# Optimization experiments

Measured on AMD Instinct MI355X. Metric: run time of the kernel, lower is better.

Reference implementation:

```python
import jax, jax.numpy as jnp
import numpy as np

D, H, F, L, V = 768, 4, 1024, 3, 10000
B, TLAB, S = 16, 513, 197
SCALE = 0.02


def setup_inputs() -> dict:
    key = jax.random.key(0)
    ks = jax.random.split(key, 16)
    inp = {
        'labels': jax.random.randint(ks[0], (B, TLAB), 0, V),
        'vision_feats': jax.random.normal(ks[1], (B, S, D), jnp.float32),
        'vis_proj_w': jax.random.normal(ks[2], (D, D), jnp.float32) * SCALE,
        'vis_proj_b': jnp.zeros((D,), jnp.float32),
        'tok_emb': jax.random.normal(ks[3], (V, D), jnp.float32) * SCALE,
        'pos_emb': jax.random.normal(ks[4], (1, 512, D), jnp.float32) * SCALE,
        'sa_w': jax.random.normal(ks[5], (L, 3 * D, D), jnp.float32) * SCALE,
        'sa_b': jnp.zeros((L, 3 * D), jnp.float32),
        'sa_out_w': jax.random.normal(ks[6], (L, D, D), jnp.float32) * SCALE,
        'sa_out_b': jnp.zeros((L, D), jnp.float32),
        'ca_w': jax.random.normal(ks[7], (L, 3 * D, D), jnp.float32) * SCALE,
        'ca_b': jnp.zeros((L, 3 * D), jnp.float32),
        'ca_out_w': jax.random.normal(ks[8], (L, D, D), jnp.float32) * SCALE,
        'ca_out_b': jnp.zeros((L, D), jnp.float32),
        'ln1_g': jnp.ones((L, D), jnp.float32), 'ln1_b': jnp.zeros((L, D), jnp.float32),
        'ln2_g': jnp.ones((L, D), jnp.float32), 'ln2_b': jnp.zeros((L, D), jnp.float32),
        'ln3_g': jnp.ones((L, D), jnp.float32), 'ln3_b': jnp.zeros((L, D), jnp.float32),
        'ff1_w': jax.random.normal(ks[9], (L, F, D), jnp.float32) * SCALE,
        'ff1_b': jnp.zeros((L, F), jnp.float32),
        'ff2_w': jax.random.normal(ks[10], (L, D, F), jnp.float32) * SCALE,
        'ff2_b': jnp.zeros((L, D), jnp.float32),
        'out_w': jax.random.normal(ks[11], (V, D), jnp.float32) * SCALE,
        'out_b': jnp.zeros((V,), jnp.float32),
    }
    return inp


def layer_norm(x, g, b, eps=1e-5):
    m = jnp.mean(x, axis=-1, keepdims=True)
    v = jnp.var(x, axis=-1, keepdims=True)
    return (x - m) / jnp.sqrt(v + eps) * g + b


def mha(qx, kx, vx, w, b, ow, ob, mask):
    # torch nn.MultiheadAttention with packed in_proj [3D, D]
    d = qx.shape[-1]
    hd = d // H
    q = qx @ w[:d].T + b[:d]
    k = kx @ w[d:2 * d].T + b[d:2 * d]
    v = vx @ w[2 * d:].T + b[2 * d:]
    def split(t):
        return t.reshape(t.shape[0], t.shape[1], H, hd).transpose(0, 2, 1, 3)
    q, k, v = split(q), split(k), split(v)  # [B,H,T,hd]
    s = jnp.einsum('bhqd,bhkd->bhqk', q, k) / jnp.sqrt(jnp.asarray(hd, qx.dtype))
    if mask is not None:
        s = s + mask
    a = jax.nn.softmax(s, axis=-1)
    o = jnp.einsum('bhqk,bhkd->bhqd', a, v)
    o = o.transpose(0, 2, 1, 3).reshape(qx.shape[0], qx.shape[1], d)
    return o @ ow.T + ob


def decode(labels, vision_feats, vis_proj_w, vis_proj_b, tok_emb, pos_emb,
           sa_w, sa_b, sa_out_w, sa_out_b, ca_w, ca_b, ca_out_w, ca_out_b,
           ln1_g, ln1_b, ln2_g, ln2_b, ln3_g, ln3_b,
           ff1_w, ff1_b, ff2_w, ff2_b, out_w, out_b):
    mem = vision_feats @ vis_proj_w.T + vis_proj_b          # [B,S,D]
    tgt_tok = labels[:, :-1]                                # [B,T] T=512
    T = tgt_tok.shape[1]
    x = tok_emb[tgt_tok] + pos_emb[:, :T, :]                # [B,T,D]
    # causal additive mask (teacher-forced loop == single full causal pass)
    mask = jnp.where(jnp.tril(jnp.ones((T, T), bool)), 0.0, -jnp.inf).astype(x.dtype)
    for l in range(L):
        x = layer_norm(x + mha(x, x, x, sa_w[l], sa_b[l], sa_out_w[l], sa_out_b[l], mask), ln1_g[l], ln1_b[l])
        x = layer_norm(x + mha(x, mem, mem, ca_w[l], ca_b[l], ca_out_w[l], ca_out_b[l], None), ln2_g[l], ln2_b[l])
        ff = jax.nn.relu(x @ ff1_w[l].T + ff1_b[l]) @ ff2_w[l].T + ff2_b[l]
        x = layer_norm(x + ff, ln3_g[l], ln3_b[l])
    return x @ out_w.T + out_b                              # [B,T,V]


def reference(labels, vision_feats, vis_proj_w, vis_proj_b, tok_emb, pos_emb,
              sa_w, sa_b, sa_out_w, sa_out_b, ca_w, ca_b, ca_out_w, ca_out_b,
              ln1_g, ln1_b, ln2_g, ln2_b, ln3_g, ln3_b,
              ff1_w, ff1_b, ff2_w, ff2_b, out_w, out_b):
    logits = decode(labels, vision_feats, vis_proj_w, vis_proj_b, tok_emb, pos_emb,
                    sa_w, sa_b, sa_out_w, sa_out_b, ca_w, ca_b, ca_out_w, ca_out_b,
                    ln1_g, ln1_b, ln2_g, ln2_b, ln3_g, ln3_b,
                    ff1_w, ff1_b, ff2_w, ff2_b, out_w, out_b)
    return (logits, labels[:, 1:])
```

## Files before the change

kernel.cpp:

```cpp
#include <hip/hip_runtime.h>
#include <hip/hip_fp8.h>

typedef unsigned short u16;
typedef __bf16 bf16x8 __attribute__((ext_vector_type(8)));
typedef float f32x4 __attribute__((ext_vector_type(4)));
typedef unsigned short u16x8 __attribute__((ext_vector_type(8)));
typedef unsigned short u16x4 __attribute__((ext_vector_type(4)));
typedef long i64;

typedef __attribute__((address_space(3))) u16 lds_u16_t;
typedef __attribute__((address_space(1))) const u16 glb_u16_t;
typedef __attribute__((address_space(3))) unsigned char lds_u8_t;
typedef __attribute__((address_space(1))) const unsigned char glb_u8_t;

__device__ __forceinline__ u16 f2bf(float f) {
    union { float f; unsigned u; } v; v.f = f;
    unsigned r = v.u + 0x7FFFu + ((v.u >> 16) & 1u);
    return (u16)(r >> 16);
}
__device__ __forceinline__ float bf2f(u16 h) {
    union { unsigned u; float f; } v; v.u = ((unsigned)h) << 16; return v.f;
}
__device__ __forceinline__ unsigned char f2e4m3(float f) {
    __hip_fp8_e4m3 h(f);
    return (unsigned char)h.__x;
}

struct CastQ { const float* s[9]; unsigned char* d[9]; long n4[9]; float mul[9]; };
__global__ __launch_bounds__(256) void castq_kernel(CastQ a) {
    int seg = blockIdx.z;
    const float* s = a.s[seg];
    unsigned char* d = a.d[seg];
    long n4 = a.n4[seg];
    float mul = a.mul[seg];
    long i = (long)blockIdx.x * 256 + threadIdx.x;
    long stride = (long)gridDim.x * 256;
    for (; i < n4; i += stride) {
        float4 f = reinterpret_cast<const float4*>(s)[i];
        uchar4 o;
        o.x = f2e4m3(f.x * mul); o.y = f2e4m3(f.y * mul);
        o.z = f2e4m3(f.z * mul); o.w = f2e4m3(f.w * mul);
        reinterpret_cast<uchar4*>(d)[i] = o;
    }
}

__global__ __launch_bounds__(256) void embed_kernel(
    const int* __restrict__ labels, const float* __restrict__ tok_emb,
    const float* __restrict__ pos_emb, u16* __restrict__ xb,
    unsigned char* __restrict__ xq, float* __restrict__ lab_out)
{
    int wid = threadIdx.x >> 6, lane = threadIdx.x & 63;
    int r = blockIdx.x * 4 + wid;
    int b = r >> 9, t = r & 511;
    int tok = labels[b * 513 + t];
    if (lane == 0) lab_out[r] = (float)labels[b * 513 + t + 1];
    const float* te = tok_emb + (long)tok * 768;
    const float* pe = pos_emb + (long)t * 768;
    u16* xo = xb + (long)r * 768;
    unsigned char* qo = xq + (long)r * 768;
    int base = lane * 12;
#pragma unroll
    for (int c = 0; c < 3; c++) {
        float4 a = *reinterpret_cast<const float4*>(te + base + c * 4);
        float4 p = *reinterpret_cast<const float4*>(pe + base + c * 4);
        float v0 = a.x + p.x, v1 = a.y + p.y, v2 = a.z + p.z, v3 = a.w + p.w;
        ushort4 o; o.x = f2bf(v0); o.y = f2bf(v1); o.z = f2bf(v2); o.w = f2bf(v3);
        *reinterpret_cast<ushort4*>(xo + base + c * 4) = o;
        uchar4 q; q.x = f2e4m3(v0); q.y = f2e4m3(v1); q.z = f2e4m3(v2); q.w = f2e4m3(v3);
        *reinterpret_cast<uchar4*>(qo + base + c * 4) = q;
    }
}

template<int OUT>
__global__ __launch_bounds__(256, 4) void gemmT(
    const u16* __restrict__ A, int lda, long sAb, long sAh,
    const u16* __restrict__ W, int ldw, long sWb, long sWh,
    void* __restrict__ C, int ldc, long sCb, long sCh,
    int M, int N, int K, int NH)
{
    __shared__ __align__(16) u16 As0[128 * 32];
    __shared__ __align__(16) u16 As1[128 * 32];
    __shared__ __align__(16) u16 Bs0[128 * 32];
    __shared__ __align__(16) u16 Bs1[128 * 32];

    int z = blockIdx.z, zb = z / NH, zh = z % NH;
    const u16* Ap = A + (long)zb * sAb + (long)zh * sAh;
    const u16* Wp = W + (long)zb * sWb + (long)zh * sWh;
    long coff = (long)zb * sCb + (long)zh * sCh;

    int gx = (int)gridDim.x, gy = (int)gridDim.y;
    int nwg = gx * gy;
    int orig = (int)(blockIdx.y * gridDim.x + blockIdx.x);
    int q = nwg >> 3, r = nwg & 7;
    int xcd = orig & 7, loc = orig >> 3;
    int wg = (xcd < r ? xcd * (q + 1) : r * (q + 1) + (xcd - r) * q) + loc;
    int full = 8 * gy;
    int nsc = (gx + 7) >> 3;
    int sc = wg / full; if (sc > nsc - 1) sc = nsc - 1;
    int rem = wg - sc * full;
    int wdt = gx - sc * 8; if (wdt > 8) wdt = 8;
    int by = rem / wdt, bx = sc * 8 + rem % wdt;

    int m0 = by * 128, n0 = bx * 128;
    int tid = threadIdx.x, wid = tid >> 6, lane = tid & 63;
    int wr = (wid >> 1) * 64, wc = (wid & 1) * 64;
    int fr = lane & 15, fk = (lane >> 4) * 8;

    int li0 = wid * 64 + lane;
    int li1 = li0 + 256;
    int r0 = li0 >> 2, c0 = (li0 & 3) * 8;
    int r1 = li1 >> 2, c1 = (li1 & 3) * 8;
    long aoff0 = (long)min(m0 + r0, M - 1) * lda + c0;
    long aoff1 = (long)min(m0 + r1, M - 1) * lda + c1;
    long woff0 = (long)min(n0 + r0, N - 1) * ldw + c0;
    long woff1 = (long)min(n0 + r1, N - 1) * ldw + c1;
    char* a0base = (char*)As0 + wid * 1024;
    char* a1base = (char*)As1 + wid * 1024;
    char* b0base = (char*)Bs0 + wid * 1024;
    char* b1base = (char*)Bs1 + wid * 1024;

    f32x4 acc[4][4] = {};

    auto stage = [&](char* ab, char* bb, int kt) {
        int k0 = kt * 32;
        __builtin_amdgcn_global_load_lds((glb_u16_t*)(Ap + aoff0 + k0), (lds_u16_t*)ab, 16, 0, 0);
        __builtin_amdgcn_global_load_lds((glb_u16_t*)(Ap + aoff1 + k0), (lds_u16_t*)(ab + 4096), 16, 0, 0);
        __builtin_amdgcn_global_load_lds((glb_u16_t*)(Wp + woff0 + k0), (lds_u16_t*)bb, 16, 0, 0);
        __builtin_amdgcn_global_load_lds((glb_u16_t*)(Wp + woff1 + k0), (lds_u16_t*)(bb + 4096), 16, 0, 0);
    };
    auto compute = [&](const u16* as, const u16* bs) {
        bf16x8 af[4], bw[4];
#pragma unroll
        for (int m = 0; m < 4; m++)
            af[m] = *reinterpret_cast<const bf16x8*>(&as[(wr + m * 16 + fr) * 32 + fk]);
#pragma unroll
        for (int n = 0; n < 4; n++)
            bw[n] = *reinterpret_cast<const bf16x8*>(&bs[(wc + n * 16 + fr) * 32 + fk]);
#pragma unroll
        for (int m = 0; m < 4; m++)
#pragma unroll
            for (int n = 0; n < 4; n++)
                acc[m][n] = __builtin_amdgcn_mfma_f32_16x16x32_bf16(af[m], bw[n], acc[m][n], 0, 0, 0);
    };

    int nt = K >> 5;
    stage(a0base, b0base, 0);
    __syncthreads();
    for (int t = 0; t < nt; t += 2) {
        stage(a1base, b1base, t + 1);
        compute(As0, Bs0);
        __syncthreads();
        if (t + 2 < nt) stage(a0base, b0base, t + 2);
        compute(As1, Bs1);
        __syncthreads();
    }

    int crow = (lane >> 4) * 4;
#pragma unroll
    for (int m = 0; m < 4; m++) {
#pragma unroll
        for (int n = 0; n < 4; n++) {
            int col = n0 + wc + n * 16 + fr;
            if (col >= N) continue;
            int rbase = m0 + wr + m * 16 + crow;
#pragma unroll
            for (int rr = 0; rr < 4; rr++) {
                int row = rbase + rr;
                if (row >= M) continue;
                float v = acc[m][n][rr];
                long idx = coff + (long)row * ldc + col;
                if (OUT == 1) ((u16*)C)[idx] = f2bf(v);
                else          ((unsigned char*)C)[idx] = f2e4m3(v);
            }
        }
    }
}

template<int OUT, int RELU, int BM, int FUSEVT>
__global__ __launch_bounds__(256, 4) void gemm8(
    const unsigned char* __restrict__ A, int lda,
    const unsigned char* __restrict__ W, int ldw,
    const float* __restrict__ bias, float outscale,
    void* __restrict__ C, int ldc, u16* __restrict__ vt,
    int M, int N, int K)
{
    constexpr int NREP = (BM == 128) ? 4 : 2;
    constexpr int AHALF = (BM == 128) ? 4096 : 2048;
    __shared__ __align__(16) unsigned char As0[BM * 64];
    __shared__ __align__(16) unsigned char As1[BM * 64];
    __shared__ __align__(16) unsigned char Bs0[128 * 64];
    __shared__ __align__(16) unsigned char Bs1[128 * 64];

    int gx = (int)gridDim.x, gy = (int)gridDim.y;
    int nwg = gx * gy;
    int orig = (int)(blockIdx.y * gridDim.x + blockIdx.x);
    int q = nwg >> 3, r = nwg & 7;
    int xcd = orig & 7, loc = orig >> 3;
    int wg = (xcd < r ? xcd * (q + 1) : r * (q + 1) + (xcd - r) * q) + loc;
    int full = 8 * gy;
    int nsc = (gx + 7) >> 3;
    int sc = wg / full; if (sc > nsc - 1) sc = nsc - 1;
    int rem = wg - sc * full;
    int wdt = gx - sc * 8; if (wdt > 8) wdt = 8;
    int by = rem / wdt, bx = sc * 8 + rem % wdt;

    int m0 = by * BM, n0 = bx * 128;
    int tid = threadIdx.x, wid = tid >> 6, lane = tid & 63;
    int wr = (BM == 128) ? (wid >> 1) * 64 : 0;
    int wc = (BM == 128) ? (wid & 1) * 64 : wid * 32;
    int fr = lane & 15, gk = (lane >> 4) * 8;

    int li0 = wid * 64 + lane;
    int rsW = li0 >> 1, csW = li0 & 1;
    int kcW = ((csW ^ (rsW >> 2)) & 1) << 4;
    long woff = (long)min(n0 + rsW, N - 1) * ldw + kcW;
    long aoff;
    if constexpr (BM == 128) {
        aoff = (long)min(m0 + rsW, M - 1) * lda + kcW;
    } else {
        int halfA = li0 >> 7;
        int rsA = (li0 >> 1) & 63, csA = li0 & 1;
        int kcA = ((csA ^ (rsA >> 2)) & 1) << 4;
        aoff = (long)min(m0 + rsA, M - 1) * lda + halfA * 32 + kcA;
    }
    char* a0base = (char*)As0 + wid * 1024;
    char* a1base = (char*)As1 + wid * 1024;
    char* b0base = (char*)Bs0 + wid * 1024;
    char* b1base = (char*)Bs1 + wid * 1024;

    f32x4 acc[4][NREP] = {};

    auto stage = [&](char* ab, char* bb, int kt) {
        int k0 = kt * 64;
        if constexpr (BM == 128) {
            __builtin_amdgcn_global_load_lds((glb_u8_t*)(A + aoff + k0), (lds_u8_t*)ab, 16, 0, 0);
            __builtin_amdgcn_global_load_lds((glb_u8_t*)(A + aoff + k0 + 32), (lds_u8_t*)(ab + 4096), 16, 0, 0);
        } else {
            __builtin_amdgcn_global_load_lds((glb_u8_t*)(A + aoff + k0), (lds_u8_t*)ab, 16, 0, 0);
        }
        __builtin_amdgcn_global_load_lds((glb_u8_t*)(W + woff + k0), (lds_u8_t*)bb, 16, 0, 0);
        __builtin_amdgcn_global_load_lds((glb_u8_t*)(W + woff + k0 + 32), (lds_u8_t*)(bb + 4096), 16, 0, 0);
    };
    int cg = gk >> 4, go = gk & 15;
    auto compute = [&](const unsigned char* as, const unsigned char* bs) {
        i64 af[4][2], bw[NREP][2];
#pragma unroll
        for (int m = 0; m < 4; m++) {
            int rr2 = wr + m * 16 + fr;
            int off = rr2 * 32 + (((cg ^ (rr2 >> 2)) & 1) << 4) + go;
            af[m][0] = *reinterpret_cast<const i64*>(as + off);
            af[m][1] = *reinterpret_cast<const i64*>(as + AHALF + off);
        }
#pragma unroll
        for (int n = 0; n < NREP; n++) {
            int rr2 = wc + n * 16 + fr;
            int off = rr2 * 32 + (((cg ^ (rr2 >> 2)) & 1) << 4) + go;
            bw[n][0] = *reinterpret_cast<const i64*>(bs + off);
            bw[n][1] = *reinterpret_cast<const i64*>(bs + 4096 + off);
        }
#pragma unroll
        for (int ks = 0; ks < 2; ks++)
#pragma unroll
            for (int m = 0; m < 4; m++)
#pragma unroll
                for (int n = 0; n < NREP; n++)
                    acc[m][n] = __builtin_amdgcn_mfma_f32_16x16x32_fp8_fp8(
                        af[m][ks], bw[n][ks], acc[m][n], 0, 0, 0);
    };

    int nt = K >> 6;
    stage(a0base, b0base, 0);
    __syncthreads();
    for (int t = 0; t < nt; t += 2) {
        stage(a1base, b1base, t + 1);
        compute(As0, Bs0);
        __syncthreads();
        if (t + 2 < nt) stage(a0base, b0base, t + 2);
        compute(As1, Bs1);
        __syncthreads();
    }

    int crow = (lane >> 4) * 4;
#pragma unroll
    for (int m = 0; m < 4; m++) {
#pragma unroll
        for (int n = 0; n < NREP; n++) {
            int col = n0 + wc + n * 16 + fr;
            if (col >= N) continue;
            float bv = bias ? bias[col] : 0.f;
            int rbase = m0 + wr + m * 16 + crow;
            float vv[4];
#pragma unroll
            for (int rr = 0; rr < 4; rr++) {
                int row = rbase + rr;
                if (row >= M) continue;
                float v = acc[m][n][rr] * outscale + bv;
                if (RELU) v = fmaxf(v, 0.f);
                vv[rr] = v;
                long idx = (long)row * ldc + col;
                if (OUT == 0)      ((float*)C)[idx] = v;
                else if (OUT == 1) ((u16*)C)[idx] = f2bf(v);
                else               ((unsigned char*)C)[idx] = f2e4m3(v);
            }
            if constexpr (FUSEVT) {
                if (col >= 1536) {
                    int tt = col - 1536;
                    int h = tt / 192, d = tt - h * 192;
                    int b = rbase >> 9, k0 = rbase & 511;
                    ushort4 o;
                    o.x = f2bf(vv[0]); o.y = f2bf(vv[1]); o.z = f2bf(vv[2]); o.w = f2bf(vv[3]);
                    *reinterpret_cast<ushort4*>(vt + ((long)((b << 2) + h) * 192 + d) * 512 + k0) = o;
                }
            }
        }
    }
}

__global__ __launch_bounds__(256) void transpose_pad(
    const u16* __restrict__ V, long sVb, long sVh, int ldv, int NH,
    u16* __restrict__ VT, long sVT, int rowsIn, int Kp)
{
    __shared__ u16 tile[32][33];
    int z = blockIdx.z, zb = z / NH, zh = z % NH;
    const u16* Vp = V + (long)zb * sVb + (long)zh * sVh;
    int k0 = blockIdx.x * 32, d0 = blockIdx.y * 32;
#pragma unroll
    for (int i = 0; i < 4; i++) {
        int k = k0 + threadIdx.y + i * 8;
        int d = d0 + threadIdx.x;
        tile[threadIdx.y + i * 8][threadIdx.x] = (k < rowsIn) ? Vp[(long)k * ldv + d] : (u16)0;
    }
    __syncthreads();
    u16* Op = VT + (long)z * sVT;
#pragma unroll
    for (int i = 0; i < 4; i++) {
        int d = d0 + threadIdx.y + i * 8;
        int k = k0 + threadIdx.x;
        Op[(long)d * Kp + k] = tile[threadIdx.x][threadIdx.y + i * 8];
    }
}

template<int CPL, int CAUSAL>
__global__ __launch_bounds__(256) void softmax2(
    const u16* __restrict__ S, u16* __restrict__ P,
    int ld_in, int valid_in, int ld_out, float scale)
{
    int wid = threadIdx.x >> 6, lane = threadIdx.x & 63;
    long r = (long)blockIdx.x * 4 + wid;
    int q = (int)(r & 511);
    int valid = CAUSAL ? (q + 1) : valid_in;
    const u16* srow = S + r * (long)ld_in;
    u16* prow = P + r * (long)ld_out;
    int base = lane * CPL;
    float v[CPL];
    if constexpr (CPL == 8) {
        u16x8 x = *reinterpret_cast<const u16x8*>(srow + base);
#pragma unroll
        for (int j = 0; j < 8; j++) v[j] = bf2f(x[j]);
    } else {
        u16x4 x = *reinterpret_cast<const u16x4*>(srow + base);
#pragma unroll
        for (int j = 0; j < 4; j++) v[j] = bf2f(x[j]);
    }
    float mx = -3e38f;
#pragma unroll
    for (int j = 0; j < CPL; j++) {
        v[j] *= scale;
        if (base + j < valid) mx = fmaxf(mx, v[j]);
    }
#pragma unroll
    for (int o = 32; o; o >>= 1) mx = fmaxf(mx, __shfl_xor(mx, o, 64));
    float e[CPL], s = 0.f;
#pragma unroll
    for (int j = 0; j < CPL; j++) {
        e[j] = (base + j < valid) ? __expf(v[j] - mx) : 0.f;
        s += e[j];
    }
#pragma unroll
    for (int o = 32; o; o >>= 1) s += __shfl_xor(s, o, 64);
    float inv = 1.f / s;
    if constexpr (CPL == 8) {
        u16x8 o8;
#pragma unroll
        for (int j = 0; j < 8; j++) o8[j] = f2bf(e[j] * inv);
        *reinterpret_cast<u16x8*>(prow + base) = o8;
    } else {
        u16x4 o4;
#pragma unroll
        for (int j = 0; j < 4; j++) o4[j] = f2bf(e[j] * inv);
        *reinterpret_cast<u16x4*>(prow + base) = o4;
    }
}

__global__ __launch_bounds__(256) void ln_kernel(
    const u16* __restrict__ xin, const u16* __restrict__ subb,
    const float* __restrict__ g, const float* __restrict__ bta,
    u16* __restrict__ xout, unsigned char* __restrict__ q8)
{
    int wid = threadIdx.x >> 6, lane = threadIdx.x & 63;
    long r = (long)blockIdx.x * 4 + wid;
    const u16* a = xin + r * 768;
    const u16* s = subb + r * 768;
    int base = lane * 12;
    float v[12];
    float sum = 0.f;
#pragma unroll
    for (int c = 0; c < 3; c++) {
        ushort4 av = *reinterpret_cast<const ushort4*>(a + base + c * 4);
        ushort4 sv = *reinterpret_cast<const ushort4*>(s + base + c * 4);
        v[c*4+0] = bf2f(av.x) + bf2f(sv.x);
        v[c*4+1] = bf2f(av.y) + bf2f(sv.y);
        v[c*4+2] = bf2f(av.z) + bf2f(sv.z);
        v[c*4+3] = bf2f(av.w) + bf2f(sv.w);
        sum += v[c*4+0] + v[c*4+1] + v[c*4+2] + v[c*4+3];
    }
#pragma unroll
    for (int o = 32; o; o >>= 1) sum += __shfl_xor(sum, o, 64);
    float mean = sum * (1.f / 768.f);
    float vs = 0.f;
#pragma unroll
    for (int j = 0; j < 12; j++) { float t = v[j] - mean; vs += t * t; }
#pragma unroll
    for (int o = 32; o; o >>= 1) vs += __shfl_xor(vs, o, 64);
    float rstd = rsqrtf(vs * (1.f / 768.f) + 1e-5f);
    u16* xo = xout + r * 768;
    unsigned char* qo = q8 + r * 768;
#pragma unroll
    for (int c = 0; c < 3; c++) {
        float4 gv = *reinterpret_cast<const float4*>(g + base + c * 4);
        float4 bv = *reinterpret_cast<const float4*>(bta + base + c * 4);
        float y0 = (v[c*4+0] - mean) * rstd * gv.x + bv.x;
        float y1 = (v[c*4+1] - mean) * rstd * gv.y + bv.y;
        float y2 = (v[c*4+2] - mean) * rstd * gv.z + bv.z;
        float y3 = (v[c*4+3] - mean) * rstd * gv.w + bv.w;
        ushort4 o; o.x = f2bf(y0); o.y = f2bf(y1); o.z = f2bf(y2); o.w = f2bf(y3);
        *reinterpret_cast<ushort4*>(xo + base + c * 4) = o;
        uchar4 qb; qb.x = f2e4m3(y0); qb.y = f2e4m3(y1); qb.z = f2e4m3(y2); qb.w = f2e4m3(y3);
        *reinterpret_cast<uchar4*>(qo + base + c * 4) = qb;
    }
}

template<int OUT>
static void gbat(hipStream_t st,
    const u16* A, int lda, long sAb, long sAh,
    const u16* W, int ldw, long sWb, long sWh,
    void* C, int ldc, long sCb, long sCh,
    int M, int N, int K, int Z, int NH) {
    dim3 g((N + 127) / 128, (M + 127) / 128, Z), b(256, 1, 1);
    gemmT<OUT><<<g,b,0,st>>>(A,lda,sAb,sAh,W,ldw,sWb,sWh,C,ldc,sCb,sCh,M,N,K,NH);
}
template<int OUT, int RELU, int BM>
static void g8(hipStream_t st, const unsigned char* A, int lda, const unsigned char* W, int ldw,
               const float* bias, void* C, int ldc, int M, int N, int K) {
    dim3 g((N + 127) / 128, (M + BM - 1) / BM, 1), b(256, 1, 1);
    gemm8<OUT,RELU,BM,0><<<g,b,0,st>>>(A,lda,W,ldw,bias,1.f/256.f,C,ldc,nullptr,M,N,K);
}
static void g8qkv(hipStream_t st, const unsigned char* A, const unsigned char* W,
                  const float* bias, u16* C, u16* vt) {
    dim3 g(18, 64, 1), b(256, 1, 1);
    gemm8<1,0,128,1><<<g,b,0,st>>>(A,768,W,768,bias,1.f/256.f,C,2304,vt,8192,2304,768);
}

extern "C" void kernel_launch(void* const* d_in, const int* in_sizes, int n_in,
                              void* d_out, int out_size, void* d_ws, size_t ws_size,
                              hipStream_t stream)
{
    const int*   labels = (const int*)  d_in[0];
    const float* vision = (const float*)d_in[1];
    const float* vpw    = (const float*)d_in[2];
    const float* vpb    = (const float*)d_in[3];
    const float* temb   = (const float*)d_in[4];
    const float* pemb   = (const float*)d_in[5];
    const float* saw    = (const float*)d_in[6];
    const float* sab    = (const float*)d_in[7];
    const float* saow   = (const float*)d_in[8];
    const float* saob   = (const float*)d_in[9];
    const float* caw    = (const float*)d_in[10];
    const float* cab    = (const float*)d_in[11];
    const float* caow   = (const float*)d_in[12];
    const float* caob   = (const float*)d_in[13];
    const float* ln1g   = (const float*)d_in[14];
    const float* ln1b   = (const float*)d_in[15];
    const float* ln2g   = (const float*)d_in[16];
    const float* ln2b   = (const float*)d_in[17];
    const float* ln3g   = (const float*)d_in[18];
    const float* ln3b   = (const float*)d_in[19];
    const float* f1w    = (const float*)d_in[20];
    const float* f1b    = (const float*)d_in[21];
    const float* f2w    = (const float*)d_in[22];
    const float* f2b    = (const float*)d_in[23];
    const float* ow     = (const float*)d_in[24];
    const float* ob     = (const float*)d_in[25];
    (void)in_sizes; (void)n_in; (void)out_size;

    char* p = (char*)d_ws;
    auto alloc = [&](long elems, int esz) -> char* {
        char* r = p; p += ((long)elems * esz + 255) & ~255L; return r;
    };
    unsigned char* w8_sa  = (unsigned char*)alloc(3L*2304*768, 1);
    unsigned char* w8_ca  = (unsigned char*)alloc(3L*2304*768, 1);
    unsigned char* w8_sao = (unsigned char*)alloc(3L*768*768, 1);
    unsigned char* w8_cao = (unsigned char*)alloc(3L*768*768, 1);
    unsigned char* w8_f1  = (unsigned char*)alloc(3L*1024*768, 1);
    unsigned char* w8_f2  = (unsigned char*)alloc(3L*768*1024, 1);
    unsigned char* w8_ow  = (unsigned char*)alloc(10000L*768, 1);
    unsigned char* w8_vp  = (unsigned char*)alloc(768L*768, 1);
    unsigned char* vis8   = (unsigned char*)alloc(3152L*768, 1);
    unsigned char* mem8   = (unsigned char*)alloc(3152L*768, 1);
    unsigned char* xq     = (unsigned char*)alloc(8192L*768, 1);
    unsigned char* h8     = (unsigned char*)alloc(8192L*1024, 1);
    unsigned char* attn8  = (unsigned char*)alloc(8192L*768, 1);
    u16* xb   = (u16*)alloc(8192L*768, 2);
    u16* qkv  = (u16*)alloc(8192L*2304, 2);
    u16* q_bf = qkv;
    u16* kv_bf = qkv + 8192L*768;
    u16* scb  = (u16*)alloc(64L*512*512, 2);
    u16* pr   = (u16*)alloc(64L*512*512, 2);
    u16* vt   = (u16*)alloc(64L*192*512, 2);
    u16* subb = (u16*)alloc(8192L*768, 2);
    if ((size_t)(p - (char*)d_ws) > ws_size) return;

    CastQ cq;
    cq.s[0] = saw;    cq.d[0] = w8_sa;  cq.n4[0] = 3L*2304*768/4;  cq.mul[0] = 256.f;
    cq.s[1] = caw;    cq.d[1] = w8_ca;  cq.n4[1] = 3L*2304*768/4;  cq.mul[1] = 256.f;
    cq.s[2] = saow;   cq.d[2] = w8_sao; cq.n4[2] = 3L*768*768/4;   cq.mul[2] = 256.f;
    cq.s[3] = caow;   cq.d[3] = w8_cao; cq.n4[3] = 3L*768*768/4;   cq.mul[3] = 256.f;
    cq.s[4] = f1w;    cq.d[4] = w8_f1;  cq.n4[4] = 3L*1024*768/4;  cq.mul[4] = 256.f;
    cq.s[5] = f2w;    cq.d[5] = w8_f2;  cq.n4[5] = 3L*768*1024/4;  cq.mul[5] = 256.f;
    cq.s[6] = ow;     cq.d[6] = w8_ow;  cq.n4[6] = 10000L*768/4;   cq.mul[6] = 256.f;
    cq.s[7] = vpw;    cq.d[7] = w8_vp;  cq.n4[7] = 768L*768/4;     cq.mul[7] = 256.f;
    cq.s[8] = vision; cq.d[8] = vis8;   cq.n4[8] = 3152L*768/4;    cq.mul[8] = 1.f;
    castq_kernel<<<dim3(512, 1, 9), dim3(256), 0, stream>>>(cq);

    embed_kernel<<<dim3(2048), dim3(256), 0, stream>>>(labels, temb, pemb, xb, xq,
                                                       (float*)d_out + 81920000L);

    g8<2,0,64>(stream, vis8, 768, w8_vp, 768, vpb, mem8, 768, 3152, 768, 768);

    const float scale = 0.07216878364870323f;

    for (int l = 0; l < 3; l++) {
        g8qkv(stream, xq, w8_sa + (long)l*2304*768, sab + l*2304, qkv, vt);
        gbat<1>(stream, qkv, 2304, 512L*2304, 192, qkv + 768, 2304, 512L*2304, 192,
                scb, 512, 4L*512*512, 512L*512, 512, 512, 192, 64, 4);
        softmax2<8,1><<<dim3(8192), dim3(256), 0, stream>>>(scb, pr, 512, 512, 512, scale);
        gbat<2>(stream, pr, 512, 4L*512*512, 512L*512, vt, 512, 4L*192*512, 192L*512,
                attn8, 768, 512L*768, 192, 512, 192, 512, 64, 4);
        g8<1,0,64>(stream, attn8, 768, w8_sao + (long)l*768*768, 768,
                   saob + l*768, subb, 768, 8192, 768, 768);
        ln_kernel<<<dim3(2048), dim3(256), 0, stream>>>(xb, subb, ln1g + l*768, ln1b + l*768,
                                                        xb, xq);

        g8<1,0,64>(stream, xq, 768, w8_ca + (long)l*2304*768, 768,
                   cab + l*2304, q_bf, 768, 8192, 768, 768);
        g8<1,0,64>(stream, mem8, 768, w8_ca + (long)l*2304*768 + 768L*768, 768,
                   cab + l*2304 + 768, kv_bf, 1536, 3152, 1536, 768);
        transpose_pad<<<dim3(8,6,64), dim3(32,8), 0, stream>>>(
            kv_bf + 768, 197L*1536, 192L, 1536, 4, vt, 192L*256, 197, 256);
        gbat<1>(stream, q_bf, 768, 512L*768, 192, kv_bf, 1536, 197L*1536, 192,
                scb, 224, 4L*512*224, 512L*224, 512, 197, 192, 64, 4);
        softmax2<4,0><<<dim3(8192), dim3(256), 0, stream>>>(scb, pr, 224, 197, 256, scale);
        gbat<2>(stream, pr, 256, 4L*512*256, 512L*256, vt, 256, 4L*192*256, 192L*256,
                attn8, 768, 512L*768, 192, 512, 192, 256, 64, 4);
        g8<1,0,64>(stream, attn8, 768, w8_cao + (long)l*768*768, 768,
                   caob + l*768, subb, 768, 8192, 768, 768);
        ln_kernel<<<dim3(2048), dim3(256), 0, stream>>>(xb, subb, ln2g + l*768, ln2b + l*768,
                                                        xb, xq);

        g8<2,1,128>(stream, xq, 768, w8_f1 + (long)l*1024*768, 768, f1b + l*1024,
                    h8, 1024, 8192, 1024, 768);
        g8<1,0,64>(stream, h8, 1024, w8_f2 + (long)l*768*1024, 1024, f2b + l*768,
                   subb, 768, 8192, 768, 1024);
        ln_kernel<<<dim3(2048), dim3(256), 0, stream>>>(xb, subb, ln3g + l*768, ln3b + l*768,
                                                        xb, xq);
    }

    g8<0,0,128>(stream, xq, 768, w8_ow, 768, ob, (float*)d_out, 10000, 8192, 10000, 768);
}
```

Baseline: 1.109 ms.

## Move attention batched GEMMs from bf16 to FP8 with scaled softmax probabilities

```diff
diff --git a/kernel.cpp b/kernel.cpp
--- a/kernel.cpp
+++ b/kernel.cpp
@@ -2,14 +2,11 @@
 #include <hip/hip_fp8.h>
 
 typedef unsigned short u16;
-typedef __bf16 bf16x8 __attribute__((ext_vector_type(8)));
 typedef float f32x4 __attribute__((ext_vector_type(4)));
 typedef unsigned short u16x8 __attribute__((ext_vector_type(8)));
 typedef unsigned short u16x4 __attribute__((ext_vector_type(4)));
 typedef long i64;
 
-typedef __attribute__((address_space(3))) u16 lds_u16_t;
-typedef __attribute__((address_space(1))) const u16 glb_u16_t;
 typedef __attribute__((address_space(3))) unsigned char lds_u8_t;
 typedef __attribute__((address_space(1))) const unsigned char glb_u8_t;
 
@@ -71,21 +68,25 @@
     }
 }
 
-template<int OUT>
-__global__ __launch_bounds__(256, 4) void gemmT(
-    const u16* __restrict__ A, int lda, long sAb, long sAh,
-    const u16* __restrict__ W, int ldw, long sWb, long sWh,
+template<int OUT, int RELU, int BM, int QKV>
+__global__ __launch_bounds__(256, 4) void gemm8(
+    const unsigned char* __restrict__ A, int lda, long sAb, long sAh,
+    const unsigned char* __restrict__ W, int ldw, long sWb, long sWh,
+    const float* __restrict__ bias, float outscale,
     void* __restrict__ C, int ldc, long sCb, long sCh,
+    unsigned char* __restrict__ vt8,
     int M, int N, int K, int NH)
 {
-    __shared__ __align__(16) u16 As0[128 * 32];
-    __shared__ __align__(16) u16 As1[128 * 32];
-    __shared__ __align__(16) u16 Bs0[128 * 32];
-    __shared__ __align__(16) u16 Bs1[128 * 32];
+    constexpr int NREP = (BM == 128) ? 4 : 2;
+    constexpr int AHALF = (BM == 128) ? 4096 : 2048;
+    __shared__ __align__(16) unsigned char As0[BM * 64];
+    __shared__ __align__(16) unsigned char As1[BM * 64];
+    __shared__ __align__(16) unsigned char Bs0[128 * 64];
+    __shared__ __align__(16) unsigned char Bs1[128 * 64];
 
     int z = blockIdx.z, zb = z / NH, zh = z % NH;
-    const u16* Ap = A + (long)zb * sAb + (long)zh * sAh;
-    const u16* Wp = W + (long)zb * sWb + (long)zh * sWh;
+    const unsigned char* Ap = A + (long)zb * sAb + (long)zh * sAh;
+    const unsigned char* Wp = W + (long)zb * sWb + (long)zh * sWh;
     long coff = (long)zb * sCb + (long)zh * sCh;
 
     int gx = (int)gridDim.x, gy = (int)gridDim.y;
@@ -101,109 +102,6 @@
     int wdt = gx - sc * 8; if (wdt > 8) wdt = 8;
     int by = rem / wdt, bx = sc * 8 + rem % wdt;
 
-    int m0 = by * 128, n0 = bx * 128;
-    int tid = threadIdx.x, wid = tid >> 6, lane = tid & 63;
-    int wr = (wid >> 1) * 64, wc = (wid & 1) * 64;
-    int fr = lane & 15, fk = (lane >> 4) * 8;
-
-    int li0 = wid * 64 + lane;
-    int li1 = li0 + 256;
-    int r0 = li0 >> 2, c0 = (li0 & 3) * 8;
-    int r1 = li1 >> 2, c1 = (li1 & 3) * 8;
-    long aoff0 = (long)min(m0 + r0, M - 1) * lda + c0;
-    long aoff1 = (long)min(m0 + r1, M - 1) * lda + c1;
-    long woff0 = (long)min(n0 + r0, N - 1) * ldw + c0;
-    long woff1 = (long)min(n0 + r1, N - 1) * ldw + c1;
-    char* a0base = (char*)As0 + wid * 1024;
-    char* a1base = (char*)As1 + wid * 1024;
-    char* b0base = (char*)Bs0 + wid * 1024;
-    char* b1base = (char*)Bs1 + wid * 1024;
-
-    f32x4 acc[4][4] = {};
-
-    auto stage = [&](char* ab, char* bb, int kt) {
-        int k0 = kt * 32;
-        __builtin_amdgcn_global_load_lds((glb_u16_t*)(Ap + aoff0 + k0), (lds_u16_t*)ab, 16, 0, 0);
-        __builtin_amdgcn_global_load_lds((glb_u16_t*)(Ap + aoff1 + k0), (lds_u16_t*)(ab + 4096), 16, 0, 0);
-        __builtin_amdgcn_global_load_lds((glb_u16_t*)(Wp + woff0 + k0), (lds_u16_t*)bb, 16, 0, 0);
-        __builtin_amdgcn_global_load_lds((glb_u16_t*)(Wp + woff1 + k0), (lds_u16_t*)(bb + 4096), 16, 0, 0);
-    };
-    auto compute = [&](const u16* as, const u16* bs) {
-        bf16x8 af[4], bw[4];
-#pragma unroll
-        for (int m = 0; m < 4; m++)
-            af[m] = *reinterpret_cast<const bf16x8*>(&as[(wr + m * 16 + fr) * 32 + fk]);
-#pragma unroll
-        for (int n = 0; n < 4; n++)
-            bw[n] = *reinterpret_cast<const bf16x8*>(&bs[(wc + n * 16 + fr) * 32 + fk]);
-#pragma unroll
-        for (int m = 0; m < 4; m++)
-#pragma unroll
-            for (int n = 0; n < 4; n++)
-                acc[m][n] = __builtin_amdgcn_mfma_f32_16x16x32_bf16(af[m], bw[n], acc[m][n], 0, 0, 0);
-    };
-
-    int nt = K >> 5;
-    stage(a0base, b0base, 0);
-    __syncthreads();
-    for (int t = 0; t < nt; t += 2) {
-        stage(a1base, b1base, t + 1);
-        compute(As0, Bs0);
-        __syncthreads();
-        if (t + 2 < nt) stage(a0base, b0base, t + 2);
-        compute(As1, Bs1);
-        __syncthreads();
-    }
-
-    int crow = (lane >> 4) * 4;
-#pragma unroll
-    for (int m = 0; m < 4; m++) {
-#pragma unroll
-        for (int n = 0; n < 4; n++) {
-            int col = n0 + wc + n * 16 + fr;
-            if (col >= N) continue;
-            int rbase = m0 + wr + m * 16 + crow;
-#pragma unroll
-            for (int rr = 0; rr < 4; rr++) {
-                int row = rbase + rr;
-                if (row >= M) continue;
-                float v = acc[m][n][rr];
-                long idx = coff + (long)row * ldc + col;
-                if (OUT == 1) ((u16*)C)[idx] = f2bf(v);
-                else          ((unsigned char*)C)[idx] = f2e4m3(v);
-            }
-        }
-    }
-}
-
-template<int OUT, int RELU, int BM, int FUSEVT>
-__global__ __launch_bounds__(256, 4) void gemm8(
-    const unsigned char* __restrict__ A, int lda,
-    const unsigned char* __restrict__ W, int ldw,
-    const float* __restrict__ bias, float outscale,
-    void* __restrict__ C, int ldc, u16* __restrict__ vt,
-    int M, int N, int K)
-{
-    constexpr int NREP = (BM == 128) ? 4 : 2;
-    constexpr int AHALF = (BM == 128) ? 4096 : 2048;
-    __shared__ __align__(16) unsigned char As0[BM * 64];
-    __shared__ __align__(16) unsigned char As1[BM * 64];
-    __shared__ __align__(16) unsigned char Bs0[128 * 64];
-    __shared__ __align__(16) unsigned char Bs1[128 * 64];
-
-    int gx = (int)gridDim.x, gy = (int)gridDim.y;
-    int nwg = gx * gy;
-    int orig = (int)(blockIdx.y * gridDim.x + blockIdx.x);
-    int q = nwg >> 3, r = nwg & 7;
-    int xcd = orig & 7, loc = orig >> 3;
-    int wg = (xcd < r ? xcd * (q + 1) : r * (q + 1) + (xcd - r) * q) + loc;
-    int full = 8 * gy;
-    int nsc = (gx + 7) >> 3;
-    int sc = wg / full; if (sc > nsc - 1) sc = nsc - 1;
-    int rem = wg - sc * full;
-    int wdt = gx - sc * 8; if (wdt > 8) wdt = 8;
-    int by = rem / wdt, bx = sc * 8 + rem % wdt;
-
     int m0 = by * BM, n0 = bx * 128;
     int tid = threadIdx.x, wid = tid >> 6, lane = tid & 63;
     int wr = (BM == 128) ? (wid >> 1) * 64 : 0;
@@ -233,13 +131,13 @@
     auto stage = [&](char* ab, char* bb, int kt) {
         int k0 = kt * 64;
         if constexpr (BM == 128) {
-            __builtin_amdgcn_global_load_lds((glb_u8_t*)(A + aoff + k0), (lds_u8_t*)ab, 16, 0, 0);
-            __builtin_amdgcn_global_load_lds((glb_u8_t*)(A + aoff + k0 + 32), (lds_u8_t*)(ab + 4096), 16, 0, 0);
+            __builtin_amdgcn_global_load_lds((glb_u8_t*)(Ap + aoff + k0), (lds_u8_t*)ab, 16, 0, 0);
+            __builtin_amdgcn_global_load_lds((glb_u8_t*)(Ap + aoff + k0 + 32), (lds_u8_t*)(ab + 4096), 16, 0, 0);
         } else {
-            __builtin_amdgcn_global_load_lds((glb_u8_t*)(A + aoff + k0), (lds_u8_t*)ab, 16, 0, 0);
+            __builtin_amdgcn_global_load_lds((glb_u8_t*)(Ap + aoff + k0), (lds_u8_t*)ab, 16, 0, 0);
         }
-        __builtin_amdgcn_global_load_lds((glb_u8_t*)(W + woff + k0), (lds_u8_t*)bb, 16, 0, 0);
-        __builtin_amdgcn_global_load_lds((glb_u8_t*)(W + woff + k0 + 32), (lds_u8_t*)(bb + 4096), 16, 0, 0);
+        __builtin_amdgcn_global_load_lds((glb_u8_t*)(Wp + woff + k0), (lds_u8_t*)bb, 16, 0, 0);
+        __builtin_amdgcn_global_load_lds((glb_u8_t*)(Wp + woff + k0 + 32), (lds_u8_t*)(bb + 4096), 16, 0, 0);
     };
     int cg = gk >> 4, go = gk & 15;
     auto compute = [&](const unsigned char* as, const unsigned char* bs) {
@@ -272,12 +170,14 @@
     stage(a0base, b0base, 0);
     __syncthreads();
     for (int t = 0; t < nt; t += 2) {
-        stage(a1base, b1base, t + 1);
+        if (t + 1 < nt) stage(a1base, b1base, t + 1);
         compute(As0, Bs0);
         __syncthreads();
-        if (t + 2 < nt) stage(a0base, b0base, t + 2);
-        compute(As1, Bs1);
-        __syncthreads();
+        if (t + 1 < nt) {
+            if (t + 2 < nt) stage(a0base, b0base, t + 2);
+            compute(As1, Bs1);
+            __syncthreads();
+        }
     }
 
     int crow = (lane >> 4) * 4;
@@ -292,46 +192,55 @@
             float vv[4];
 #pragma unroll
             for (int rr = 0; rr < 4; rr++) {
-                int row = rbase + rr;
-                if (row >= M) continue;
                 float v = acc[m][n][rr] * outscale + bv;
                 if (RELU) v = fmaxf(v, 0.f);
                 vv[rr] = v;
-                long idx = (long)row * ldc + col;
-                if (OUT == 0)      ((float*)C)[idx] = v;
-                else if (OUT == 1) ((u16*)C)[idx] = f2bf(v);
-                else               ((unsigned char*)C)[idx] = f2e4m3(v);
             }
-            if constexpr (FUSEVT) {
-                if (col >= 1536) {
+            if constexpr (QKV) {
+                if (col < 1536) {
+#pragma unroll
+                    for (int rr = 0; rr < 4; rr++)
+                        ((unsigned char*)C)[coff + (long)(rbase + rr) * ldc + col] = f2e4m3(vv[rr]);
+                } else {
                     int tt = col - 1536;
                     int h = tt / 192, d = tt - h * 192;
                     int b = rbase >> 9, k0 = rbase & 511;
-                    ushort4 o;
-                    o.x = f2bf(vv[0]); o.y = f2bf(vv[1]); o.z = f2bf(vv[2]); o.w = f2bf(vv[3]);
-                    *reinterpret_cast<ushort4*>(vt + ((long)((b << 2) + h) * 192 + d) * 512 + k0) = o;
+                    uchar4 o;
+                    o.x = f2e4m3(vv[0]); o.y = f2e4m3(vv[1]);
+                    o.z = f2e4m3(vv[2]); o.w = f2e4m3(vv[3]);
+                    *reinterpret_cast<uchar4*>(vt8 + ((long)((b << 2) + h) * 192 + d) * 512 + k0) = o;
+                }
+            } else {
+#pragma unroll
+                for (int rr = 0; rr < 4; rr++) {
+                    int row = rbase + rr;
+                    if (row >= M) continue;
+                    long idx = coff + (long)row * ldc + col;
+                    if (OUT == 0)      ((float*)C)[idx] = vv[rr];
+                    else if (OUT == 1) ((u16*)C)[idx] = f2bf(vv[rr]);
+                    else               ((unsigned char*)C)[idx] = f2e4m3(vv[rr]);
                 }
             }
         }
     }
 }
 
-__global__ __launch_bounds__(256) void transpose_pad(
-    const u16* __restrict__ V, long sVb, long sVh, int ldv, int NH,
-    u16* __restrict__ VT, long sVT, int rowsIn, int Kp)
-{
-    __shared__ u16 tile[32][33];
+__global__ __launch_bounds__(256) void transpose_pad8(
+    const unsigned char* __restrict__ V, long sVb, long sVh, int ldv, int NH,
+    unsigned char* __restrict__ VT, long sVT, int rowsIn, int Kp)
+{
+    __shared__ unsigned char tile[32][33];
     int z = blockIdx.z, zb = z / NH, zh = z % NH;
-    const u16* Vp = V + (long)zb * sVb + (long)zh * sVh;
+    const unsigned char* Vp = V + (long)zb * sVb + (long)zh * sVh;
     int k0 = blockIdx.x * 32, d0 = blockIdx.y * 32;
 #pragma unroll
     for (int i = 0; i < 4; i++) {
         int k = k0 + threadIdx.y + i * 8;
         int d = d0 + threadIdx.x;
-        tile[threadIdx.y + i * 8][threadIdx.x] = (k < rowsIn) ? Vp[(long)k * ldv + d] : (u16)0;
+        tile[threadIdx.y + i * 8][threadIdx.x] = (k < rowsIn) ? Vp[(long)k * ldv + d] : (unsigned char)0;
     }
     __syncthreads();
-    u16* Op = VT + (long)z * sVT;
+    unsigned char* Op = VT + (long)z * sVT;
 #pragma unroll
     for (int i = 0; i < 4; i++) {
         int d = d0 + threadIdx.y + i * 8;
@@ -342,7 +251,7 @@
 
 template<int CPL, int CAUSAL>
 __global__ __launch_bounds__(256) void softmax2(
-    const u16* __restrict__ S, u16* __restrict__ P,
+    const u16* __restrict__ S, unsigned char* __restrict__ P,
     int ld_in, int valid_in, int ld_out, float scale)
 {
     int wid = threadIdx.x >> 6, lane = threadIdx.x & 63;
@@ -350,7 +259,7 @@
     int q = (int)(r & 511);
     int valid = CAUSAL ? (q + 1) : valid_in;
     const u16* srow = S + r * (long)ld_in;
-    u16* prow = P + r * (long)ld_out;
+    unsigned char* prow = P + r * (long)ld_out;
     int base = lane * CPL;
     float v[CPL];
     if constexpr (CPL == 8) {
@@ -378,17 +287,17 @@
     }
 #pragma unroll
     for (int o = 32; o; o >>= 1) s += __shfl_xor(s, o, 64);
-    float inv = 1.f / s;
+    float inv = 64.f / s;
     if constexpr (CPL == 8) {
-        u16x8 o8;
-#pragma unroll
-        for (int j = 0; j < 8; j++) o8[j] = f2bf(e[j] * inv);
-        *reinterpret_cast<u16x8*>(prow + base) = o8;
+        union { unsigned char b[8]; i64 v8; } o;
+#pragma unroll
+        for (int j = 0; j < 8; j++) o.b[j] = f2e4m3(e[j] * inv);
+        *reinterpret_cast<i64*>(prow + base) = o.v8;
     } else {
-        u16x4 o4;
-#pragma unroll
-        for (int j = 0; j < 4; j++) o4[j] = f2bf(e[j] * inv);
-        *reinterpret_cast<u16x4*>(prow + base) = o4;
+        uchar4 o4;
+        o4.x = f2e4m3(e[0] * inv); o4.y = f2e4m3(e[1] * inv);
+        o4.z = f2e4m3(e[2] * inv); o4.w = f2e4m3(e[3] * inv);
+        *reinterpret_cast<uchar4*>(prow + base) = o4;
     }
 }
 
@@ -440,25 +349,27 @@
     }
 }
 
-template<int OUT>
-static void gbat(hipStream_t st,
-    const u16* A, int lda, long sAb, long sAh,
-    const u16* W, int ldw, long sWb, long sWh,
-    void* C, int ldc, long sCb, long sCh,
-    int M, int N, int K, int Z, int NH) {
-    dim3 g((N + 127) / 128, (M + 127) / 128, Z), b(256, 1, 1);
-    gemmT<OUT><<<g,b,0,st>>>(A,lda,sAb,sAh,W,ldw,sWb,sWh,C,ldc,sCb,sCh,M,N,K,NH);
-}
 template<int OUT, int RELU, int BM>
 static void g8(hipStream_t st, const unsigned char* A, int lda, const unsigned char* W, int ldw,
                const float* bias, void* C, int ldc, int M, int N, int K) {
     dim3 g((N + 127) / 128, (M + BM - 1) / BM, 1), b(256, 1, 1);
-    gemm8<OUT,RELU,BM,0><<<g,b,0,st>>>(A,lda,W,ldw,bias,1.f/256.f,C,ldc,nullptr,M,N,K);
+    gemm8<OUT,RELU,BM,0><<<g,b,0,st>>>(A,lda,0,0,W,ldw,0,0,bias,1.f/256.f,C,ldc,0,0,nullptr,M,N,K,1);
+}
+template<int OUT>
+static void g8bat(hipStream_t st,
+    const unsigned char* A, int lda, long sAb, long sAh,
+    const unsigned char* W, int ldw, long sWb, long sWh,
+    float outscale, void* C, int ldc, long sCb, long sCh,
+    int M, int N, int K, int Z, int NH) {
+    dim3 g((N + 127) / 128, (M + 127) / 128, Z), b(256, 1, 1);
+    gemm8<OUT,0,128,0><<<g,b,0,st>>>(A,lda,sAb,sAh,W,ldw,sWb,sWh,nullptr,outscale,
+                                     C,ldc,sCb,sCh,nullptr,M,N,K,NH);
 }
 static void g8qkv(hipStream_t st, const unsigned char* A, const unsigned char* W,
-                  const float* bias, u16* C, u16* vt) {
+                  const float* bias, unsigned char* q8k8, unsigned char* vt8) {
     dim3 g(18, 64, 1), b(256, 1, 1);
-    gemm8<1,0,128,1><<<g,b,0,st>>>(A,768,W,768,bias,1.f/256.f,C,2304,vt,8192,2304,768);
+    gemm8<2,0,128,1><<<g,b,0,st>>>(A,768,0,0,W,768,0,0,bias,1.f/256.f,
+                                   q8k8,1536,0,0,vt8,8192,2304,768,1);
 }
 
 extern "C" void kernel_launch(void* const* d_in, const int* in_sizes, int n_in,
@@ -510,13 +421,13 @@
     unsigned char* xq     = (unsigned char*)alloc(8192L*768, 1);
     unsigned char* h8     = (unsigned char*)alloc(8192L*1024, 1);
     unsigned char* attn8  = (unsigned char*)alloc(8192L*768, 1);
+    unsigned char* q8k8   = (unsigned char*)alloc(8192L*1536, 1);
+    unsigned char* q8ca   = (unsigned char*)alloc(8192L*768, 1);
+    unsigned char* kv8    = (unsigned char*)alloc(3152L*1536, 1);
+    unsigned char* vt8    = (unsigned char*)alloc(64L*192*512, 1);
+    unsigned char* pr8    = (unsigned char*)alloc(64L*512*512, 1);
     u16* xb   = (u16*)alloc(8192L*768, 2);
-    u16* qkv  = (u16*)alloc(8192L*2304, 2);
-    u16* q_bf = qkv;
-    u16* kv_bf = qkv + 8192L*768;
     u16* scb  = (u16*)alloc(64L*512*512, 2);
-    u16* pr   = (u16*)alloc(64L*512*512, 2);
-    u16* vt   = (u16*)alloc(64L*192*512, 2);
     u16* subb = (u16*)alloc(8192L*768, 2);
     if ((size_t)(p - (char*)d_ws) > ws_size) return;
 
@@ -538,30 +449,31 @@
     g8<2,0,64>(stream, vis8, 768, w8_vp, 768, vpb, mem8, 768, 3152, 768, 768);
 
     const float scale = 0.07216878364870323f;
+    const float PSCALE_INV = 1.f / 64.f;
 
     for (int l = 0; l < 3; l++) {
-        g8qkv(stream, xq, w8_sa + (long)l*2304*768, sab + l*2304, qkv, vt);
-        gbat<1>(stream, qkv, 2304, 512L*2304, 192, qkv + 768, 2304, 512L*2304, 192,
-                scb, 512, 4L*512*512, 512L*512, 512, 512, 192, 64, 4);
-        softmax2<8,1><<<dim3(8192), dim3(256), 0, stream>>>(scb, pr, 512, 512, 512, scale);
-        gbat<2>(stream, pr, 512, 4L*512*512, 512L*512, vt, 512, 4L*192*512, 192L*512,
-                attn8, 768, 512L*768, 192, 512, 192, 512, 64, 4);
+        g8qkv(stream, xq, w8_sa + (long)l*2304*768, sab + l*2304, q8k8, vt8);
+        g8bat<1>(stream, q8k8, 1536, 512L*1536, 192, q8k8 + 768, 1536, 512L*1536, 192,
+                 1.f, scb, 512, 4L*512*512, 512L*512, 512, 512, 192, 64, 4);
+        softmax2<8,1><<<dim3(8192), dim3(256), 0, stream>>>(scb, pr8, 512, 512, 512, scale);
+        g8bat<2>(stream, pr8, 512, 4L*512*512, 512L*512, vt8, 512, 4L*192*512, 192L*512,
+                 PSCALE_INV, attn8, 768, 512L*768, 192, 512, 192, 512, 64, 4);
         g8<1,0,64>(stream, attn8, 768, w8_sao + (long)l*768*768, 768,
                    saob + l*768, subb, 768, 8192, 768, 768);
         ln_kernel<<<dim3(2048), dim3(256), 0, stream>>>(xb, subb, ln1g + l*768, ln1b + l*768,
                                                         xb, xq);
 
-        g8<1,0,64>(stream, xq, 768, w8_ca + (long)l*2304*768, 768,
-                   cab + l*2304, q_bf, 768, 8192, 768, 768);
-        g8<1,0,64>(stream, mem8, 768, w8_ca + (long)l*2304*768 + 768L*768, 768,
-                   cab + l*2304 + 768, kv_bf, 1536, 3152, 1536, 768);
-        transpose_pad<<<dim3(8,6,64), dim3(32,8), 0, stream>>>(
-            kv_bf + 768, 197L*1536, 192L, 1536, 4, vt, 192L*256, 197, 256);
-        gbat<1>(stream, q_bf, 768, 512L*768, 192, kv_bf, 1536, 197L*1536, 192,
-                scb, 224, 4L*512*224, 512L*224, 512, 197, 192, 64, 4);
-        softmax2<4,0><<<dim3(8192), dim3(256), 0, stream>>>(scb, pr, 224, 197, 256, scale);
-        gbat<2>(stream, pr, 256, 4L*512*256, 512L*256, vt, 256, 4L*192*256, 192L*256,
-                attn8, 768, 512L*768, 192, 512, 192, 256, 64, 4);
+        g8<2,0,64>(stream, xq, 768, w8_ca + (long)l*2304*768, 768,
+                   cab + l*2304, q8ca, 768, 8192, 768, 768);
+        g8<2,0,64>(stream, mem8, 768, w8_ca + (long)l*2304*768 + 768L*768, 768,
+                   cab + l*2304 + 768, kv8, 1536, 3152, 1536, 768);
+        transpose_pad8<<<dim3(8,6,64), dim3(32,8), 0, stream>>>(
+            kv8 + 768, 197L*1536, 192L, 1536, 4, vt8, 192L*256, 197, 256);
+        g8bat<1>(stream, q8ca, 768, 512L*768, 192, kv8, 1536, 197L*1536, 192,
+                 1.f, scb, 224, 4L*512*224, 512L*224, 512, 197, 192, 64, 4);
+        softmax2<4,0><<<dim3(8192), dim3(256), 0, stream>>>(scb, pr8, 224, 197, 256, scale);
+        g8bat<2>(stream, pr8, 256, 4L*512*256, 512L*256, vt8, 256, 4L*192*256, 192L*256,
+                 PSCALE_INV, attn8, 768, 512L*768, 192, 512, 192, 256, 64, 4);
         g8<1,0,64>(stream, attn8, 768, w8_cao + (long)l*768*768, 768,
                    caob + l*768, subb, 768, 8192, 768, 768);
         ln_kernel<<<dim3(2048), dim3(256), 0, stream>>>(xb, subb, ln2g + l*768, ln2b + l*768,
```

Result: faster. 1.067 ms (-3.7%).
